# Kernel tuning notes

Hardware: AMD Instinct MI355X
Metric: run time of the kernel (lower is better)

The kernel has to match this reference:

```python
import jax, jax.numpy as jnp
import numpy as np

CLIP = 1.0e6
TRANSITION_JITTER = 1.0e-4
CHOLESKY_JITTER = 1.0e-5
MAX_NLL_PER_STEP = 1.0e4
LOG_2PI = float(np.log(2.0 * np.pi))
T, NUM_SITES, NUM_COMPONENTS = 512, 128, 2
D = NUM_SITES * NUM_COMPONENTS


def _symmetrize(m):
    return 0.5 * (m + m.swapaxes(-1, -2))


def _sanitize_operator(m):
    m = jnp.nan_to_num(m, nan=0.0, posinf=CLIP, neginf=-CLIP)
    return jnp.clip(m, -CLIP, CLIP)


def _sanitize_symmetric(m):
    return _symmetrize(_sanitize_operator(m))


def _sanitize_vector(v):
    v = jnp.nan_to_num(v, nan=0.0, posinf=CLIP, neginf=-CLIP)
    return jnp.clip(v, -CLIP, CLIP)


def setup_inputs() -> dict:
    key = jax.random.key(0)
    ks = jax.random.split(key, 8)
    eye = jnp.eye(D, dtype=jnp.float32)
    # Stable per-step transition: near-identity with small learned-kernel-like perturbation.
    transition = 0.9 * eye + (0.05 / np.sqrt(D)) * jax.random.normal(ks[0], (T, D, D), dtype=jnp.float32)
    forcing = 0.1 * jax.random.normal(ks[1], (T, D), dtype=jnp.float32)
    observations = jax.random.normal(ks[2], (T, D), dtype=jnp.float32)
    # PSD process / measurement covariances (SeparableCrossCovariance outputs are PSD).
    a = jax.random.normal(ks[3], (D, D), dtype=jnp.float32) / np.sqrt(D)
    process_cov = 0.01 * (a @ a.T) + 0.05 * eye
    b = jax.random.normal(ks[4], (D, D), dtype=jnp.float32) / np.sqrt(D)
    measurement_cov = 0.01 * (b @ b.T) + 0.1 * eye
    initial_mean = jax.random.normal(ks[5], (D,), dtype=jnp.float32)
    initial_cov_diag = 0.5 + jax.random.uniform(ks[6], (D,), dtype=jnp.float32)
    return {
        "observations": observations,
        "transition": transition,
        "forcing": forcing,
        "process_cov": process_cov,
        "measurement_cov": measurement_cov,
        "initial_mean": initial_mean,
        "initial_cov_diag": initial_cov_diag,
    }


def reference(observations, transition, forcing, process_cov, measurement_cov, initial_mean, initial_cov_diag):
    dt = observations.dtype
    d = observations.shape[-1]
    eye = jnp.eye(d, dtype=dt)
    Q = _sanitize_symmetric(process_cov) + TRANSITION_JITTER * eye
    R = _sanitize_symmetric(measurement_cov)
    m0 = _sanitize_vector(initial_mean)
    P0 = jnp.diag(jnp.clip(initial_cov_diag, 1e-6, CLIP))

    def step(carry, inp):
        m, P = carry
        A_t, f_t, y_t = inp
        A_t = _sanitize_operator(A_t)
        f_t = _sanitize_vector(f_t)
        # predict
        pred_m = A_t @ m + f_t
        pred_P = _symmetrize(A_t @ P @ A_t.T) + Q
        # innovation (identity measurement operator)
        S = _symmetrize(pred_P + R) + CHOLESKY_JITTER * eye
        L = jnp.linalg.cholesky(S)
        innov = y_t - pred_m
        alpha = jax.scipy.linalg.cho_solve((L, True), innov)      # S^{-1} innov
        K = jax.scipy.linalg.cho_solve((L, True), pred_P).T       # pred_P S^{-1}
        new_m = pred_m + K @ innov
        new_P = _symmetrize((eye - K) @ pred_P)
        logdet = 2.0 * jnp.sum(jnp.log(jnp.diagonal(L)))
        nll_t = 0.5 * (innov @ alpha + logdet + d * LOG_2PI)
        nll_t = jnp.minimum(nll_t, MAX_NLL_PER_STEP)
        return (new_m, new_P), (pred_m, new_m, nll_t)

    (_, _), (pred_means, filt_means, nlls) = jax.lax.scan(
        step, (m0, P0), (transition, forcing, observations)
    )
    return jnp.sum(nlls), filt_means, pred_means
```

## Files before the change

### kernel.cpp

```cpp
#include <hip/hip_runtime.h>
#include <math.h>

#define NWG   65
#define DIM   256
#define LDM   260
#define TSTEPS 512
#define CLIPV 1.0e6f
#define TJIT  1.0e-4f
#define CJIT  1.0e-5f
#define MAXNLL 1.0e4f
#define LOG2PI 1.8378770664093453f

#define OFF_P    0
#define OFF_AP   66560
#define OFF_PP   133120
#define OFF_S    199680
#define OFF_L    266240
#define OFF_GT   332800
#define OFF_SY   399620
#define OFF_Q    466180
#define OFF_R    532740
#define OFF_VEC  599300

__device__ float    g_ws[600832];
__device__ unsigned g_bar[2];
__device__ unsigned g_broken;

__device__ __forceinline__ void gbar() {
    __syncthreads();
    if (threadIdx.x == 0) {
        if (__hip_atomic_load(&g_broken, __ATOMIC_RELAXED, __HIP_MEMORY_SCOPE_AGENT) == 0u) {
            __threadfence();
            unsigned g = __hip_atomic_load(&g_bar[1], __ATOMIC_SEQ_CST, __HIP_MEMORY_SCOPE_AGENT);
            unsigned a = __hip_atomic_fetch_add(&g_bar[0], 1u, __ATOMIC_SEQ_CST, __HIP_MEMORY_SCOPE_AGENT);
            if (a == (unsigned)(NWG - 1)) {
                __hip_atomic_store(&g_bar[0], 0u, __ATOMIC_SEQ_CST, __HIP_MEMORY_SCOPE_AGENT);
                __hip_atomic_fetch_add(&g_bar[1], 1u, __ATOMIC_SEQ_CST, __HIP_MEMORY_SCOPE_AGENT);
            } else {
                int spins = 0;
                while (__hip_atomic_load(&g_bar[1], __ATOMIC_SEQ_CST, __HIP_MEMORY_SCOPE_AGENT) == g) {
                    __builtin_amdgcn_s_sleep(2);
                    if (++spins > 2000000) {
                        __hip_atomic_store(&g_broken, 1u, __ATOMIC_RELAXED, __HIP_MEMORY_SCOPE_AGENT);
                        break;
                    }
                }
            }
            __threadfence();
        }
    }
    __syncthreads();
}

__device__ __forceinline__ float fsan(float x) {
    x = isnan(x) ? 0.0f : x;
    return fminf(fmaxf(x, -CLIPV), CLIPV);
}
__device__ __forceinline__ float rdlane(float v, int l) {
    return __int_as_float(__builtin_amdgcn_readlane(__float_as_int(v), l));
}
__device__ __forceinline__ float wave_sum(float v) {
    #pragma unroll
    for (int off = 32; off; off >>= 1) v += __shfl_xor(v, off, 64);
    return v;
}

__device__ void chol64(const float* src, int sstride, float* Lm, float* rdiag, int b0) {
    const int lane = threadIdx.x & 63;
    float a[64];
    const float* srow = src + (size_t)lane * sstride;
    #pragma unroll
    for (int k = 0; k < 64; k += 4) {
        float4 v = *(const float4*)(srow + k);
        a[k] = v.x; a[k+1] = v.y; a[k+2] = v.z; a[k+3] = v.w;
    }
    float rdv = 0.0f;
    #pragma unroll
    for (int j = 0; j < 64; ++j) {
        float d  = rdlane(a[j], j);
        float sq = sqrtf(d);
        float rs = 1.0f / sq;
        if (lane == j) rdv = rs;
        if (lane >= j) a[j] *= rs;
        float ljrs = a[j] * rs;
        #pragma unroll
        for (int k = j + 1; k < 64; ++k) {
            float skj = rdlane(a[k], j);
            if (lane > j) a[k] = fmaf(-ljrs, skj, a[k]);
        }
    }
    float* lrow = Lm + (size_t)(b0 + lane) * LDM + b0;
    #pragma unroll
    for (int k = 0; k < 64; k += 4) {
        float4 v; v.x = a[k]; v.y = a[k+1]; v.z = a[k+2]; v.w = a[k+3];
        *(float4*)(lrow + k) = v;
    }
    rdiag[b0 + lane] = rdv;
}

__device__ void trsm_col_wave(const float* Sm, float* Lm, const float* rdiag, int b0, int c) {
    const int lane = threadIdx.x & 63;
    float b   = Sm[(size_t)c * LDM + b0 + lane];
    float rdl = rdiag[b0 + lane];
    float x   = 0.0f;
    const float* lbase = Lm + (size_t)(b0 + lane) * LDM + b0;
    for (int i0 = 0; i0 < 64; i0 += 4) {
        float4 lv = *(const float4*)(lbase + i0);
        #pragma unroll
        for (int s = 0; s < 4; ++s) {
            int i = i0 + s;
            float xi = rdlane(b, i) * rdlane(rdl, i);
            x = (lane == i) ? xi : x;
            float lvi = (s == 0) ? lv.x : (s == 1) ? lv.y : (s == 2) ? lv.z : lv.w;
            b = fmaf(-lvi, xi, b);
        }
    }
    Lm[(size_t)c * LDM + b0 + lane] = x;
}

__device__ void gsolve_wave(const float* PPm, const float* innov, float* GT,
                            const float* Lm, const float* rdiag, int c) {
    const int lane = threadIdx.x & 63;
    float b[4], x[4], rd[4];
    const float* lp[4];
    #pragma unroll
    for (int q = 0; q < 4; ++q) {
        int r = lane + 64 * q;
        b[q]  = (c < 256) ? PPm[(size_t)c * LDM + r] : innov[r];
        x[q]  = 0.0f;
        rd[q] = rdiag[r];
        lp[q] = Lm + (size_t)r * LDM;
    }
    #pragma unroll
    for (int q = 0; q < 4; ++q) {
        for (int ii0 = 0; ii0 < 64; ii0 += 4) {
            float4 a0 = *(const float4*)(lp[0] + q * 64 + ii0);
            float4 a1 = *(const float4*)(lp[1] + q * 64 + ii0);
            float4 a2 = *(const float4*)(lp[2] + q * 64 + ii0);
            float4 a3 = *(const float4*)(lp[3] + q * 64 + ii0);
            #pragma unroll
            for (int s = 0; s < 4; ++s) {
                int il = ii0 + s;
                float xi = rdlane(b[q], il) * rdlane(rd[q], il);
                x[q] = (lane == il) ? xi : x[q];
                float c0 = (s==0)?a0.x:(s==1)?a0.y:(s==2)?a0.z:a0.w;
                float c1 = (s==0)?a1.x:(s==1)?a1.y:(s==2)?a1.z:a1.w;
                float c2 = (s==0)?a2.x:(s==1)?a2.y:(s==2)?a2.z:a2.w;
                float c3 = (s==0)?a3.x:(s==1)?a3.y:(s==2)?a3.z:a3.w;
                b[0] = fmaf(-c0, xi, b[0]);
                b[1] = fmaf(-c1, xi, b[1]);
                b[2] = fmaf(-c2, xi, b[2]);
                b[3] = fmaf(-c3, xi, b[3]);
            }
        }
    }
    #pragma unroll
    for (int q = 0; q < 4; ++q) GT[(size_t)c * LDM + lane + 64 * q] = x[q];
}

__device__ void block_update64(float* Sm, const float* Lm, float* smem, int b1, int b0, int tid) {
    float* Ls = smem;
    for (int e = tid; e < 64 * 64; e += 256) {
        int r = e >> 6, k = e & 63;
        Ls[r * 66 + k] = Lm[(size_t)(b1 + r) * LDM + b0 + k];
    }
    __syncthreads();
    int tx = tid & 15, ty = tid >> 4;
    int r0 = 4 * ty, c0 = 4 * tx;
    float acc[4][4] = {};
    for (int k = 0; k < 64; ++k) {
        float xr[4], yc[4];
        #pragma unroll
        for (int q = 0; q < 4; ++q) { xr[q] = Ls[(r0+q)*66 + k]; yc[q] = Ls[(c0+q)*66 + k]; }
        #pragma unroll
        for (int r = 0; r < 4; ++r)
            #pragma unroll
            for (int cc = 0; cc < 4; ++cc) acc[r][cc] = fmaf(xr[r], yc[cc], acc[r][cc]);
    }
    __syncthreads();
    #pragma unroll
    for (int r = 0; r < 4; ++r)
        #pragma unroll
        for (int cc = 0; cc < 4; ++cc)
            Sm[(size_t)(b1 + r0 + r) * LDM + b1 + c0 + cc] -= acc[r][cc];
}

__device__ void trailing_tiles(float* Sm, const float* Lm, float* smem,
                               int rb, int nt, int b0, int wg, int tid) {
    int cnt = 0;
    for (int ti = 0; ti < nt; ++ti) {
        for (int tj = 0; tj <= ti; ++tj) {
            if (ti < 2 && tj < 2) continue;
            if ((cnt++ & 63) != wg) continue;
            int i0 = rb + 32 * ti, j0 = rb + 32 * tj;
            float* Xs = smem;
            float* Ys = smem + 32 * 66;
            for (int e = tid; e < 32 * 64; e += 256) {
                int r = e >> 6, k = e & 63;
                Xs[r * 66 + k] = Lm[(size_t)(i0 + r) * LDM + b0 + k];
                Ys[r * 66 + k] = Lm[(size_t)(j0 + r) * LDM + b0 + k];
            }
            __syncthreads();
            int tx = tid & 15, ty = tid >> 4;
            int r0 = 2 * ty, c0 = 2 * tx;
            float a00 = 0, a01 = 0, a10 = 0, a11 = 0;
            #pragma unroll 4
            for (int k = 0; k < 64; ++k) {
                float x0 = Xs[r0*66 + k], x1 = Xs[(r0+1)*66 + k];
                float y0 = Ys[c0*66 + k], y1 = Ys[(c0+1)*66 + k];
                a00 = fmaf(x0, y0, a00); a01 = fmaf(x0, y1, a01);
                a10 = fmaf(x1, y0, a10); a11 = fmaf(x1, y1, a11);
            }
            __syncthreads();
            int gi = i0 + r0, gj = j0 + c0;
            Sm[(size_t)gi * LDM + gj]           -= a00;
            Sm[(size_t)gi * LDM + gj + 1]       -= a01;
            Sm[(size_t)(gi + 1) * LDM + gj]     -= a10;
            Sm[(size_t)(gi + 1) * LDM + gj + 1] -= a11;
            if (ti != tj) {
                Sm[(size_t)gj * LDM + gi]           -= a00;
                Sm[(size_t)gj * LDM + gi + 1]       -= a10;
                Sm[(size_t)(gj + 1) * LDM + gi]     -= a01;
                Sm[(size_t)(gj + 1) * LDM + gi + 1] -= a11;
            }
        }
    }
}

__global__ __launch_bounds__(256, 1) void kf_kernel(
    const float* __restrict__ obs, const float* __restrict__ trans,
    const float* __restrict__ forc, const float* __restrict__ proc,
    const float* __restrict__ meas, const float* __restrict__ im,
    const float* __restrict__ icd, float* __restrict__ out)
{
    __shared__ float smem[4608];

    const int wg   = blockIdx.x;
    const int tid  = threadIdx.x;
    const int lane = tid & 63;
    const int wv   = tid >> 6;
    const int gw   = wg * 4 + wv;

    float* Pm  = g_ws + OFF_P;
    float* AP  = g_ws + OFF_AP;
    float* PPm = g_ws + OFF_PP;
    float* Sm  = g_ws + OFF_S;
    float* Lm  = g_ws + OFF_L;
    float* GT  = g_ws + OFF_GT;
    float* SY  = g_ws + OFF_SY;
    float* Qm  = g_ws + OFF_Q;
    float* Rm  = g_ws + OFF_R;
    float* vec = g_ws + OFF_VEC;
    float* mvec  = vec;
    float* predm = vec + 256;
    float* innov = vec + 512;
    float* gtz   = vec + 768;
    float* rdiag = vec + 1024;
    float* scal  = vec + 1280;

    float* out_filt = out + 1;
    float* out_pred = out + 1 + TSTEPS * DIM;

    for (int e = wg * 256 + tid; e < DIM * DIM; e += NWG * 256) {
        int i = e >> 8, j = e & 255;
        float q = 0.5f * (fsan(proc[i * 256 + j]) + fsan(proc[j * 256 + i])) + (i == j ? TJIT : 0.0f);
        Qm[(size_t)i * LDM + j] = q;
        Rm[(size_t)i * LDM + j] = 0.5f * (fsan(meas[i * 256 + j]) + fsan(meas[j * 256 + i]));
        Pm[(size_t)i * LDM + j] = (i == j) ? fminf(fmaxf(icd[i], 1e-6f), CLIPV) : 0.0f;
    }
    if (wg == 64) {
        mvec[tid] = fsan(im[tid]);
        gtz[tid]  = 0.0f;
        if (tid < 3) scal[tid] = 0.0f;
    }
    gbar();

    for (int t = 0; t < TSTEPS; ++t) {
        const float* At = trans + (size_t)t * DIM * DIM;

        if (wg < 64) {
            int ti = wg >> 3, tj = wg & 7, i0 = ti * 32, j0 = tj * 32;
            int tx = tid & 15, ty = tid >> 4;
            int r0 = 2 * ty, c0 = 2 * tx;
            float a00 = 0, a01 = 0, a10 = 0, a11 = 0;
            float* As = smem;
            float* Bs = smem + 32 * 66;
            for (int kc = 0; kc < 256; kc += 64) {
                for (int e = tid; e < 32 * 64; e += 256) {
                    int r = e >> 6, k = e & 63;
                    As[r * 66 + k] = fsan(At[(i0 + r) * 256 + kc + k]);
                }
                for (int e = tid; e < 64 * 32; e += 256) {
                    int k = e >> 5, c = e & 31;
                    Bs[k * 34 + c] = Pm[(size_t)(kc + k) * LDM + j0 + c];
                }
                __syncthreads();
                #pragma unroll 8
                for (int k = 0; k < 64; ++k) {
                    float x0 = As[r0*66 + k], x1 = As[(r0+1)*66 + k];
                    float y0 = Bs[k*34 + c0], y1 = Bs[k*34 + c0 + 1];
                    a00 = fmaf(x0, y0, a00); a01 = fmaf(x0, y1, a01);
                    a10 = fmaf(x1, y0, a10); a11 = fmaf(x1, y1, a11);
                }
                __syncthreads();
            }
            AP[(size_t)(i0 + r0) * LDM + j0 + c0]         = a00;
            AP[(size_t)(i0 + r0) * LDM + j0 + c0 + 1]     = a01;
            AP[(size_t)(i0 + r0 + 1) * LDM + j0 + c0]     = a10;
            AP[(size_t)(i0 + r0 + 1) * LDM + j0 + c0 + 1] = a11;
        } else if (t > 0) {
            float nm = predm[tid] + gtz[tid];
            mvec[tid] = nm;
            out_filt[(size_t)(t - 1) * DIM + tid] = nm;
            if (tid == 0) {
                float nll = 0.5f * (scal[0] + scal[1] + 256.0f * LOG2PI);
                scal[2] += fminf(nll, MAXNLL);
            }
        }
        gbar();

        if (wg < 64) {
            int ti = wg >> 3, tj = wg & 7, i0 = ti * 32, j0 = tj * 32;
            int tx = tid & 15, ty = tid >> 4;
            int r0 = 2 * ty, c0 = 2 * tx;
            float a00 = 0, a01 = 0, a10 = 0, a11 = 0;
            float* Xs = smem;
            float* Ys = smem + 32 * 66;
            for (int kc = 0; kc < 256; kc += 64) {
                for (int e = tid; e < 32 * 64; e += 256) {
                    int r = e >> 6, k = e & 63;
                    Xs[r * 66 + k] = AP[(size_t)(i0 + r) * LDM + kc + k];
                    Ys[r * 66 + k] = fsan(At[(j0 + r) * 256 + kc + k]);
                }
                __syncthreads();
                #pragma unroll 8
                for (int k = 0; k < 64; ++k) {
                    float x0 = Xs[r0*66 + k], x1 = Xs[(r0+1)*66 + k];
                    float y0 = Ys[c0*66 + k], y1 = Ys[(c0+1)*66 + k];
                    a00 = fmaf(x0, y0, a00); a01 = fmaf(x0, y1, a01);
                    a10 = fmaf(x1, y0, a10); a11 = fmaf(x1, y1, a11);
                }
                __syncthreads();
            }
            SY[(size_t)(i0 + r0) * LDM + j0 + c0]         = a00;
            SY[(size_t)(i0 + r0) * LDM + j0 + c0 + 1]     = a01;
            SY[(size_t)(i0 + r0 + 1) * LDM + j0 + c0]     = a10;
            SY[(size_t)(i0 + r0 + 1) * LDM + j0 + c0 + 1] = a11;
        }
        gbar();

        if (gw < 256) {
            int r = gw;
            float s = 0.0f;
            #pragma unroll
            for (int q = 0; q < 4; ++q)
                s = fmaf(fsan(At[r * 256 + lane + 64 * q]), mvec[lane + 64 * q], s);
            s = wave_sum(s);
            if (lane == 0) {
                float pm = s + fsan(forc[(size_t)t * DIM + r]);
                predm[r] = pm;
                innov[r] = obs[(size_t)t * DIM + r] - pm;
                out_pred[(size_t)t * DIM + r] = pm;
            }
        }
        if (wg < 64) {
            for (int e = wg * 256 + tid; e < DIM * DIM; e += 64 * 256) {
                int i = e >> 8, j = e & 255;
                float sy = 0.5f * (SY[(size_t)i * LDM + j] + SY[(size_t)j * LDM + i]);
                float pp = sy + Qm[(size_t)i * LDM + j];
                PPm[(size_t)i * LDM + j] = pp;
                Sm[(size_t)i * LDM + j]  = pp + Rm[(size_t)i * LDM + j] + (i == j ? CJIT : 0.0f);
            }
        } else {
            float* Ss = smem;
            for (int e = tid; e < 64 * 64; e += 256) {
                int i = e >> 6, j = e & 63;
                float sy = 0.5f * (SY[(size_t)i * LDM + j] + SY[(size_t)j * LDM + i]);
                Ss[i * 68 + j] = sy + Qm[(size_t)i * LDM + j] + Rm[(size_t)i * LDM + j]
                                 + (i == j ? CJIT : 0.0f);
            }
            __syncthreads();
            if (wv == 0) chol64(Ss, 68, Lm, rdiag, 0);
        }
        gbar();

        if (gw < 192) trsm_col_wave(Sm, Lm, rdiag, 0, 64 + gw);
        gbar();

        if (wg == 64) {
            block_update64(Sm, Lm, smem, 64, 0, tid);
            __syncthreads();
            if (wv == 0) chol64(Sm + (size_t)64 * LDM + 64, LDM, Lm, rdiag, 64);
        } else {
            trailing_tiles(Sm, Lm, smem, 64, 6, 0, wg, tid);
        }
        gbar();

        if (gw < 128) trsm_col_wave(Sm, Lm, rdiag, 64, 128 + gw);
        gbar();

        if (wg == 64) {
            block_update64(Sm, Lm, smem, 128, 64, tid);
            __syncthreads();
            if (wv == 0) chol64(Sm + (size_t)128 * LDM + 128, LDM, Lm, rdiag, 128);
        } else {
            trailing_tiles(Sm, Lm, smem, 128, 4, 64, wg, tid);
        }
        gbar();

        if (gw < 64) trsm_col_wave(Sm, Lm, rdiag, 128, 192 + gw);
        gbar();

        if (wg == 64) {
            block_update64(Sm, Lm, smem, 192, 128, tid);
            __syncthreads();
            if (wv == 0) chol64(Sm + (size_t)192 * LDM + 192, LDM, Lm, rdiag, 192);
        }
        gbar();

        if (gw < 257) gsolve_wave(PPm, innov, GT, Lm, rdiag, gw);
        gbar();

        if (wg < 36) {
            int cnt = 0, ti = 0, tj = 0;
            for (int a = 0; a < 8; ++a)
                for (int b2 = 0; b2 <= a; ++b2) {
                    if (cnt == wg) { ti = a; tj = b2; }
                    ++cnt;
                }
            int i0 = ti * 32, j0 = tj * 32;
            int tx = tid & 15, ty = tid >> 4;
            int r0 = 2 * ty, c0 = 2 * tx;
            float a00 = 0, a01 = 0, a10 = 0, a11 = 0;
            float* Xs = smem;
            float* Ys = smem + 32 * 66;
            for (int kc = 0; kc < 256; kc += 64) {
                for (int e = tid; e < 32 * 64; e += 256) {
                    int r = e >> 6, k = e & 63;
                    Xs[r * 66 + k] = GT[(size_t)(i0 + r) * LDM + kc + k];
                    Ys[r * 66 + k] = GT[(size_t)(j0 + r) * LDM + kc + k];
                }
                __syncthreads();
                #pragma unroll 8
                for (int k = 0; k < 64; ++k) {
                    float x0 = Xs[r0*66 + k], x1 = Xs[(r0+1)*66 + k];
                    float y0 = Ys[c0*66 + k], y1 = Ys[(c0+1)*66 + k];
                    a00 = fmaf(x0, y0, a00); a01 = fmaf(x0, y1, a01);
                    a10 = fmaf(x1, y0, a10); a11 = fmaf(x1, y1, a11);
                }
                __syncthreads();
            }
            int gi = i0 + r0, gj = j0 + c0;
            float v00 = PPm[(size_t)gi * LDM + gj]           - a00;
            float v01 = PPm[(size_t)gi * LDM + gj + 1]       - a01;
            float v10 = PPm[(size_t)(gi + 1) * LDM + gj]     - a10;
            float v11 = PPm[(size_t)(gi + 1) * LDM + gj + 1] - a11;
            Pm[(size_t)gi * LDM + gj]           = v00;
            Pm[(size_t)gi * LDM + gj + 1]       = v01;
            Pm[(size_t)(gi + 1) * LDM + gj]     = v10;
            Pm[(size_t)(gi + 1) * LDM + gj + 1] = v11;
            if (ti != tj) {
                Pm[(size_t)gj * LDM + gi]           = v00;
                Pm[(size_t)gj * LDM + gi + 1]       = v10;
                Pm[(size_t)(gj + 1) * LDM + gi]     = v01;
                Pm[(size_t)(gj + 1) * LDM + gi + 1] = v11;
            }
        } else if (wg < 64) {
            for (int r = gw - 144; r < 256; r += 112) {
                float s = 0.0f;
                #pragma unroll
                for (int q = 0; q < 4; ++q)
                    s = fmaf(GT[(size_t)r * LDM + lane + 64 * q],
                             GT[(size_t)256 * LDM + lane + 64 * q], s);
                s = wave_sum(s);
                if (lane == 0) gtz[r] = s;
            }
        } else {
            if (wv == 0) {
                float s = 0.0f;
                #pragma unroll
                for (int q = 0; q < 4; ++q) {
                    float z = GT[(size_t)256 * LDM + lane + 64 * q];
                    s = fmaf(z, z, s);
                }
                s = wave_sum(s);
                if (lane == 0) scal[0] = s;
            } else if (wv == 1) {
                float s = 0.0f;
                #pragma unroll
                for (int q = 0; q < 4; ++q) s += logf(rdiag[lane + 64 * q]);
                s = wave_sum(s);
                if (lane == 0) scal[1] = -2.0f * s;
            }
        }
        gbar();
    }

    if (wg == 64) {
        float nm = predm[tid] + gtz[tid];
        out_filt[(size_t)511 * DIM + tid] = nm;
        if (tid == 0) {
            float nll = fminf(0.5f * (scal[0] + scal[1] + 256.0f * LOG2PI), MAXNLL);
            out[0] = scal[2] + nll;
            if (__hip_atomic_load(&g_broken, __ATOMIC_RELAXED, __HIP_MEMORY_SCOPE_AGENT) != 0u)
                out[0] = -1.2345678e7f;
        }
    }
}

extern "C" void kernel_launch(void* const* d_in, const int* in_sizes, int n_in,
                              void* d_out, int out_size, void* d_ws, size_t ws_size,
                              hipStream_t stream) {
    (void)in_sizes; (void)n_in; (void)out_size; (void)d_ws; (void)ws_size;
    const float* obs  = (const float*)d_in[0];
    const float* trn  = (const float*)d_in[1];
    const float* forc = (const float*)d_in[2];
    const float* proc = (const float*)d_in[3];
    const float* meas = (const float*)d_in[4];
    const float* im   = (const float*)d_in[5];
    const float* icd  = (const float*)d_in[6];
    float* out = (float*)d_out;

    kf_kernel<<<dim3(NWG), dim3(256), 0, stream>>>(obs, trn, forc, proc, meas, im, icd, out);
}
```

Measured before the change: 157.7 ms.

## Restructure Kalman step: fewer grid barriers, single-block Cholesky, flag-based barrier

Cuts the grid from 65 blocks of 256 threads to 33 blocks of 512. The counter barrier becomes per-block generation flags that every block polls. The A·P·Aᵀ and symmetrize/add stages are fused into one pass that computes both products per tile, and the predicted-mean step is folded into the last block during the A·P phase. The blocked Cholesky, TRSM and trailing updates now run entirely inside one block with __syncthreads instead of grid barriers. This removes many grid-wide barriers per timestep. The cost is serialising the factorisation onto a single CU and having more threads poll flags at each barrier.

```diff
diff --git a/kernel.cpp b/kernel.cpp
--- a/kernel.cpp
+++ b/kernel.cpp
@@ -1,7 +1,9 @@
 #include <hip/hip_runtime.h>
 #include <math.h>
 
-#define NWG   65
+#define NWG   33
+#define NT    512
+#define CHOLW 32
 #define DIM   256
 #define LDM   260
 #define TSTEPS 512
@@ -17,39 +19,36 @@
 #define OFF_S    199680
 #define OFF_L    266240
 #define OFF_GT   332800
-#define OFF_SY   399620
-#define OFF_Q    466180
-#define OFF_R    532740
-#define OFF_VEC  599300
-
-__device__ float    g_ws[600832];
-__device__ unsigned g_bar[2];
+#define OFF_Q    399620
+#define OFF_R    466180
+#define OFF_VEC  532740
+
+__device__ __align__(16) float g_ws[534276];
+struct __align__(128) BarFlag { unsigned v; unsigned pad[31]; };
+__device__ BarFlag g_flags[NWG];
 __device__ unsigned g_broken;
 
-__device__ __forceinline__ void gbar() {
+__device__ __forceinline__ void gbar(unsigned gen) {
     __syncthreads();
     if (threadIdx.x == 0) {
-        if (__hip_atomic_load(&g_broken, __ATOMIC_RELAXED, __HIP_MEMORY_SCOPE_AGENT) == 0u) {
-            __threadfence();
-            unsigned g = __hip_atomic_load(&g_bar[1], __ATOMIC_SEQ_CST, __HIP_MEMORY_SCOPE_AGENT);
-            unsigned a = __hip_atomic_fetch_add(&g_bar[0], 1u, __ATOMIC_SEQ_CST, __HIP_MEMORY_SCOPE_AGENT);
-            if (a == (unsigned)(NWG - 1)) {
-                __hip_atomic_store(&g_bar[0], 0u, __ATOMIC_SEQ_CST, __HIP_MEMORY_SCOPE_AGENT);
-                __hip_atomic_fetch_add(&g_bar[1], 1u, __ATOMIC_SEQ_CST, __HIP_MEMORY_SCOPE_AGENT);
-            } else {
-                int spins = 0;
-                while (__hip_atomic_load(&g_bar[1], __ATOMIC_SEQ_CST, __HIP_MEMORY_SCOPE_AGENT) == g) {
-                    __builtin_amdgcn_s_sleep(2);
-                    if (++spins > 2000000) {
-                        __hip_atomic_store(&g_broken, 1u, __ATOMIC_RELAXED, __HIP_MEMORY_SCOPE_AGENT);
-                        break;
-                    }
-                }
-            }
-            __threadfence();
+        __threadfence();
+        __hip_atomic_store(&g_flags[blockIdx.x].v, gen, __ATOMIC_RELEASE, __HIP_MEMORY_SCOPE_AGENT);
+    }
+    if (threadIdx.x < NWG) {
+        int spins = 0;
+        while (__hip_atomic_load(&g_flags[threadIdx.x].v, __ATOMIC_ACQUIRE, __HIP_MEMORY_SCOPE_AGENT) < gen) {
+            __builtin_amdgcn_s_sleep(1);
+            if (++spins > 4000000) {
+                __hip_atomic_store(&g_broken, 1u, __ATOMIC_RELAXED, __HIP_MEMORY_SCOPE_AGENT);
+                break;
+            }
+            if ((spins & 2047) == 0 &&
+                __hip_atomic_load(&g_broken, __ATOMIC_RELAXED, __HIP_MEMORY_SCOPE_AGENT) != 0u)
+                break;
         }
     }
     __syncthreads();
+    __threadfence();
 }
 
 __device__ __forceinline__ float fsan(float x) {
@@ -65,6 +64,7 @@
     return v;
 }
 
+__attribute__((noinline))
 __device__ void chol64(const float* src, int sstride, float* Lm, float* rdiag, int b0) {
     const int lane = threadIdx.x & 63;
     float a[64];
@@ -78,15 +78,13 @@
     #pragma unroll
     for (int j = 0; j < 64; ++j) {
         float d  = rdlane(a[j], j);
-        float sq = sqrtf(d);
-        float rs = 1.0f / sq;
+        float rs = 1.0f / sqrtf(d);
         if (lane == j) rdv = rs;
         if (lane >= j) a[j] *= rs;
-        float ljrs = a[j] * rs;
         #pragma unroll
         for (int k = j + 1; k < 64; ++k) {
-            float skj = rdlane(a[k], j);
-            if (lane > j) a[k] = fmaf(-ljrs, skj, a[k]);
+            float lkj = rdlane(a[j], k);
+            if (lane > j) a[k] = fmaf(-a[j], lkj, a[k]);
         }
     }
     float* lrow = Lm + (size_t)(b0 + lane) * LDM + b0;
@@ -158,88 +156,59 @@
     for (int q = 0; q < 4; ++q) GT[(size_t)c * LDM + lane + 64 * q] = x[q];
 }
 
-__device__ void block_update64(float* Sm, const float* Lm, float* smem, int b1, int b0, int tid) {
-    float* Ls = smem;
-    for (int e = tid; e < 64 * 64; e += 256) {
-        int r = e >> 6, k = e & 63;
-        Ls[r * 66 + k] = Lm[(size_t)(b1 + r) * LDM + b0 + k];
-    }
-    __syncthreads();
-    int tx = tid & 15, ty = tid >> 4;
-    int r0 = 4 * ty, c0 = 4 * tx;
+__device__ void trail_tile_wave(float* Sm, const float* Lm, int i0, int j0, int b0) {
+    const int lane = threadIdx.x & 63;
+    const int ly = lane >> 3, lx = lane & 7;
     float acc[4][4] = {};
-    for (int k = 0; k < 64; ++k) {
-        float xr[4], yc[4];
-        #pragma unroll
-        for (int q = 0; q < 4; ++q) { xr[q] = Ls[(r0+q)*66 + k]; yc[q] = Ls[(c0+q)*66 + k]; }
+    for (int kk = 0; kk < 64; kk += 4) {
+        float4 xv[4], yv[4];
+        #pragma unroll
+        for (int r = 0; r < 4; ++r)
+            xv[r] = *(const float4*)(Lm + (size_t)(i0 + 4*ly + r) * LDM + b0 + kk);
+        #pragma unroll
+        for (int c = 0; c < 4; ++c)
+            yv[c] = *(const float4*)(Lm + (size_t)(j0 + 4*lx + c) * LDM + b0 + kk);
         #pragma unroll
         for (int r = 0; r < 4; ++r)
             #pragma unroll
-            for (int cc = 0; cc < 4; ++cc) acc[r][cc] = fmaf(xr[r], yc[cc], acc[r][cc]);
-    }
-    __syncthreads();
+            for (int c = 0; c < 4; ++c) {
+                acc[r][c] = fmaf(xv[r].x, yv[c].x, acc[r][c]);
+                acc[r][c] = fmaf(xv[r].y, yv[c].y, acc[r][c]);
+                acc[r][c] = fmaf(xv[r].z, yv[c].z, acc[r][c]);
+                acc[r][c] = fmaf(xv[r].w, yv[c].w, acc[r][c]);
+            }
+    }
     #pragma unroll
     for (int r = 0; r < 4; ++r)
         #pragma unroll
-        for (int cc = 0; cc < 4; ++cc)
-            Sm[(size_t)(b1 + r0 + r) * LDM + b1 + c0 + cc] -= acc[r][cc];
-}
-
-__device__ void trailing_tiles(float* Sm, const float* Lm, float* smem,
-                               int rb, int nt, int b0, int wg, int tid) {
-    int cnt = 0;
-    for (int ti = 0; ti < nt; ++ti) {
-        for (int tj = 0; tj <= ti; ++tj) {
-            if (ti < 2 && tj < 2) continue;
-            if ((cnt++ & 63) != wg) continue;
-            int i0 = rb + 32 * ti, j0 = rb + 32 * tj;
-            float* Xs = smem;
-            float* Ys = smem + 32 * 66;
-            for (int e = tid; e < 32 * 64; e += 256) {
-                int r = e >> 6, k = e & 63;
-                Xs[r * 66 + k] = Lm[(size_t)(i0 + r) * LDM + b0 + k];
-                Ys[r * 66 + k] = Lm[(size_t)(j0 + r) * LDM + b0 + k];
-            }
-            __syncthreads();
-            int tx = tid & 15, ty = tid >> 4;
-            int r0 = 2 * ty, c0 = 2 * tx;
-            float a00 = 0, a01 = 0, a10 = 0, a11 = 0;
-            #pragma unroll 4
-            for (int k = 0; k < 64; ++k) {
-                float x0 = Xs[r0*66 + k], x1 = Xs[(r0+1)*66 + k];
-                float y0 = Ys[c0*66 + k], y1 = Ys[(c0+1)*66 + k];
-                a00 = fmaf(x0, y0, a00); a01 = fmaf(x0, y1, a01);
-                a10 = fmaf(x1, y0, a10); a11 = fmaf(x1, y1, a11);
-            }
-            __syncthreads();
-            int gi = i0 + r0, gj = j0 + c0;
-            Sm[(size_t)gi * LDM + gj]           -= a00;
-            Sm[(size_t)gi * LDM + gj + 1]       -= a01;
-            Sm[(size_t)(gi + 1) * LDM + gj]     -= a10;
-            Sm[(size_t)(gi + 1) * LDM + gj + 1] -= a11;
-            if (ti != tj) {
-                Sm[(size_t)gj * LDM + gi]           -= a00;
-                Sm[(size_t)gj * LDM + gi + 1]       -= a10;
-                Sm[(size_t)(gj + 1) * LDM + gi]     -= a01;
-                Sm[(size_t)(gj + 1) * LDM + gi + 1] -= a11;
-            }
-        }
-    }
-}
-
-__global__ __launch_bounds__(256, 1) void kf_kernel(
+        for (int c = 0; c < 4; ++c)
+            Sm[(size_t)(i0 + 4*ly + r) * LDM + j0 + 4*lx + c] -= acc[r][c];
+}
+
+__device__ void trail_panel(float* Sm, const float* Lm, int rb, int nt, int b0, int wv) {
+    const int cnt = nt * (nt + 1) / 2;
+    for (int idx = wv; idx < cnt; idx += 8) {
+        int ti = 0, tj = 0;
+        for (int a = 0, s = 0; a < nt; ++a) {
+            if (idx < s + a + 1) { ti = a; tj = idx - s; break; }
+            s += a + 1;
+        }
+        trail_tile_wave(Sm, Lm, rb + 32 * ti, rb + 32 * tj, b0);
+    }
+}
+
+__global__ __launch_bounds__(NT, 2) void kf_kernel(
     const float* __restrict__ obs, const float* __restrict__ trans,
     const float* __restrict__ forc, const float* __restrict__ proc,
     const float* __restrict__ meas, const float* __restrict__ im,
     const float* __restrict__ icd, float* __restrict__ out)
 {
-    __shared__ float smem[4608];
+    __shared__ float smem[8576];
 
     const int wg   = blockIdx.x;
     const int tid  = threadIdx.x;
     const int lane = tid & 63;
     const int wv   = tid >> 6;
-    const int gw   = wg * 4 + wv;
 
     float* Pm  = g_ws + OFF_P;
     float* AP  = g_ws + OFF_AP;
@@ -247,7 +216,6 @@
     float* Sm  = g_ws + OFF_S;
     float* Lm  = g_ws + OFF_L;
     float* GT  = g_ws + OFF_GT;
-    float* SY  = g_ws + OFF_SY;
     float* Qm  = g_ws + OFF_Q;
     float* Rm  = g_ws + OFF_R;
     float* vec = g_ws + OFF_VEC;
@@ -261,44 +229,47 @@
     float* out_filt = out + 1;
     float* out_pred = out + 1 + TSTEPS * DIM;
 
-    for (int e = wg * 256 + tid; e < DIM * DIM; e += NWG * 256) {
+    unsigned gen = __hip_atomic_load(&g_flags[blockIdx.x].v, __ATOMIC_RELAXED, __HIP_MEMORY_SCOPE_AGENT);
+
+    for (int e = wg * NT + tid; e < DIM * DIM; e += NWG * NT) {
         int i = e >> 8, j = e & 255;
-        float q = 0.5f * (fsan(proc[i * 256 + j]) + fsan(proc[j * 256 + i])) + (i == j ? TJIT : 0.0f);
-        Qm[(size_t)i * LDM + j] = q;
+        Qm[(size_t)i * LDM + j] = 0.5f * (fsan(proc[i * 256 + j]) + fsan(proc[j * 256 + i]))
+                                  + (i == j ? TJIT : 0.0f);
         Rm[(size_t)i * LDM + j] = 0.5f * (fsan(meas[i * 256 + j]) + fsan(meas[j * 256 + i]));
         Pm[(size_t)i * LDM + j] = (i == j) ? fminf(fmaxf(icd[i], 1e-6f), CLIPV) : 0.0f;
     }
-    if (wg == 64) {
+    if (wg == CHOLW && tid < 256) {
         mvec[tid] = fsan(im[tid]);
         gtz[tid]  = 0.0f;
         if (tid < 3) scal[tid] = 0.0f;
     }
-    gbar();
+    gbar(++gen);
 
     for (int t = 0; t < TSTEPS; ++t) {
         const float* At = trans + (size_t)t * DIM * DIM;
 
-        if (wg < 64) {
-            int ti = wg >> 3, tj = wg & 7, i0 = ti * 32, j0 = tj * 32;
-            int tx = tid & 15, ty = tid >> 4;
-            int r0 = 2 * ty, c0 = 2 * tx;
+        if (wg < 32) {
+            const int ti = wg >> 2, tj = wg & 3;
+            const int i0 = ti * 32, j0 = tj * 64;
+            const int ty = tid >> 5, tx = tid & 31;
+            const int r0 = 2 * ty, c0 = 2 * tx;
             float a00 = 0, a01 = 0, a10 = 0, a11 = 0;
             float* As = smem;
-            float* Bs = smem + 32 * 66;
+            float* Bs = smem + 32 * 68;
             for (int kc = 0; kc < 256; kc += 64) {
-                for (int e = tid; e < 32 * 64; e += 256) {
+                for (int e = tid; e < 32 * 64; e += NT) {
                     int r = e >> 6, k = e & 63;
-                    As[r * 66 + k] = fsan(At[(i0 + r) * 256 + kc + k]);
-                }
-                for (int e = tid; e < 64 * 32; e += 256) {
-                    int k = e >> 5, c = e & 31;
-                    Bs[k * 34 + c] = Pm[(size_t)(kc + k) * LDM + j0 + c];
+                    As[r * 68 + k] = fsan(At[(i0 + r) * 256 + kc + k]);
+                }
+                for (int e = tid; e < 64 * 64; e += NT) {
+                    int r = e >> 6, c = e & 63;
+                    Bs[r * 68 + c] = Pm[(size_t)(kc + r) * LDM + j0 + c];
                 }
                 __syncthreads();
                 #pragma unroll 8
                 for (int k = 0; k < 64; ++k) {
-                    float x0 = As[r0*66 + k], x1 = As[(r0+1)*66 + k];
-                    float y0 = Bs[k*34 + c0], y1 = Bs[k*34 + c0 + 1];
+                    float x0 = As[r0 * 68 + k], x1 = As[(r0 + 1) * 68 + k];
+                    float y0 = Bs[k * 68 + c0], y1 = Bs[k * 68 + c0 + 1];
                     a00 = fmaf(x0, y0, a00); a01 = fmaf(x0, y1, a01);
                     a10 = fmaf(x1, y0, a10); a11 = fmaf(x1, y1, a11);
                 }
@@ -308,179 +279,161 @@
             AP[(size_t)(i0 + r0) * LDM + j0 + c0 + 1]     = a01;
             AP[(size_t)(i0 + r0 + 1) * LDM + j0 + c0]     = a10;
             AP[(size_t)(i0 + r0 + 1) * LDM + j0 + c0 + 1] = a11;
-        } else if (t > 0) {
-            float nm = predm[tid] + gtz[tid];
-            mvec[tid] = nm;
-            out_filt[(size_t)(t - 1) * DIM + tid] = nm;
-            if (tid == 0) {
-                float nll = 0.5f * (scal[0] + scal[1] + 256.0f * LOG2PI);
-                scal[2] += fminf(nll, MAXNLL);
-            }
-        }
-        gbar();
-
-        if (wg < 64) {
-            int ti = wg >> 3, tj = wg & 7, i0 = ti * 32, j0 = tj * 32;
-            int tx = tid & 15, ty = tid >> 4;
-            int r0 = 2 * ty, c0 = 2 * tx;
-            float a00 = 0, a01 = 0, a10 = 0, a11 = 0;
-            float* Xs = smem;
-            float* Ys = smem + 32 * 66;
-            for (int kc = 0; kc < 256; kc += 64) {
-                for (int e = tid; e < 32 * 64; e += 256) {
-                    int r = e >> 6, k = e & 63;
-                    Xs[r * 66 + k] = AP[(size_t)(i0 + r) * LDM + kc + k];
-                    Ys[r * 66 + k] = fsan(At[(j0 + r) * 256 + kc + k]);
-                }
-                __syncthreads();
-                #pragma unroll 8
-                for (int k = 0; k < 64; ++k) {
-                    float x0 = Xs[r0*66 + k], x1 = Xs[(r0+1)*66 + k];
-                    float y0 = Ys[c0*66 + k], y1 = Ys[(c0+1)*66 + k];
-                    a00 = fmaf(x0, y0, a00); a01 = fmaf(x0, y1, a01);
-                    a10 = fmaf(x1, y0, a10); a11 = fmaf(x1, y1, a11);
-                }
-                __syncthreads();
-            }
-            SY[(size_t)(i0 + r0) * LDM + j0 + c0]         = a00;
-            SY[(size_t)(i0 + r0) * LDM + j0 + c0 + 1]     = a01;
-            SY[(size_t)(i0 + r0 + 1) * LDM + j0 + c0]     = a10;
-            SY[(size_t)(i0 + r0 + 1) * LDM + j0 + c0 + 1] = a11;
-        }
-        gbar();
-
-        if (gw < 256) {
-            int r = gw;
-            float s = 0.0f;
-            #pragma unroll
-            for (int q = 0; q < 4; ++q)
-                s = fmaf(fsan(At[r * 256 + lane + 64 * q]), mvec[lane + 64 * q], s);
-            s = wave_sum(s);
-            if (lane == 0) {
-                float pm = s + fsan(forc[(size_t)t * DIM + r]);
-                predm[r] = pm;
-                innov[r] = obs[(size_t)t * DIM + r] - pm;
-                out_pred[(size_t)t * DIM + r] = pm;
-            }
-        }
-        if (wg < 64) {
-            for (int e = wg * 256 + tid; e < DIM * DIM; e += 64 * 256) {
-                int i = e >> 8, j = e & 255;
-                float sy = 0.5f * (SY[(size_t)i * LDM + j] + SY[(size_t)j * LDM + i]);
-                float pp = sy + Qm[(size_t)i * LDM + j];
-                PPm[(size_t)i * LDM + j] = pp;
-                Sm[(size_t)i * LDM + j]  = pp + Rm[(size_t)i * LDM + j] + (i == j ? CJIT : 0.0f);
-            }
         } else {
-            float* Ss = smem;
-            for (int e = tid; e < 64 * 64; e += 256) {
-                int i = e >> 6, j = e & 63;
-                float sy = 0.5f * (SY[(size_t)i * LDM + j] + SY[(size_t)j * LDM + i]);
-                Ss[i * 68 + j] = sy + Qm[(size_t)i * LDM + j] + Rm[(size_t)i * LDM + j]
-                                 + (i == j ? CJIT : 0.0f);
-            }
-            __syncthreads();
-            if (wv == 0) chol64(Ss, 68, Lm, rdiag, 0);
-        }
-        gbar();
-
-        if (gw < 192) trsm_col_wave(Sm, Lm, rdiag, 0, 64 + gw);
-        gbar();
-
-        if (wg == 64) {
-            block_update64(Sm, Lm, smem, 64, 0, tid);
-            __syncthreads();
-            if (wv == 0) chol64(Sm + (size_t)64 * LDM + 64, LDM, Lm, rdiag, 64);
-        } else {
-            trailing_tiles(Sm, Lm, smem, 64, 6, 0, wg, tid);
-        }
-        gbar();
-
-        if (gw < 128) trsm_col_wave(Sm, Lm, rdiag, 64, 128 + gw);
-        gbar();
-
-        if (wg == 64) {
-            block_update64(Sm, Lm, smem, 128, 64, tid);
-            __syncthreads();
-            if (wv == 0) chol64(Sm + (size_t)128 * LDM + 128, LDM, Lm, rdiag, 128);
-        } else {
-            trailing_tiles(Sm, Lm, smem, 128, 4, 64, wg, tid);
-        }
-        gbar();
-
-        if (gw < 64) trsm_col_wave(Sm, Lm, rdiag, 128, 192 + gw);
-        gbar();
-
-        if (wg == 64) {
-            block_update64(Sm, Lm, smem, 192, 128, tid);
-            __syncthreads();
-            if (wv == 0) chol64(Sm + (size_t)192 * LDM + 192, LDM, Lm, rdiag, 192);
-        }
-        gbar();
-
-        if (gw < 257) gsolve_wave(PPm, innov, GT, Lm, rdiag, gw);
-        gbar();
-
-        if (wg < 36) {
-            int cnt = 0, ti = 0, tj = 0;
-            for (int a = 0; a < 8; ++a)
-                for (int b2 = 0; b2 <= a; ++b2) {
-                    if (cnt == wg) { ti = a; tj = b2; }
-                    ++cnt;
-                }
-            int i0 = ti * 32, j0 = tj * 32;
-            int tx = tid & 15, ty = tid >> 4;
-            int r0 = 2 * ty, c0 = 2 * tx;
-            float a00 = 0, a01 = 0, a10 = 0, a11 = 0;
-            float* Xs = smem;
-            float* Ys = smem + 32 * 66;
-            for (int kc = 0; kc < 256; kc += 64) {
-                for (int e = tid; e < 32 * 64; e += 256) {
-                    int r = e >> 6, k = e & 63;
-                    Xs[r * 66 + k] = GT[(size_t)(i0 + r) * LDM + kc + k];
-                    Ys[r * 66 + k] = GT[(size_t)(j0 + r) * LDM + kc + k];
-                }
-                __syncthreads();
-                #pragma unroll 8
-                for (int k = 0; k < 64; ++k) {
-                    float x0 = Xs[r0*66 + k], x1 = Xs[(r0+1)*66 + k];
-                    float y0 = Ys[c0*66 + k], y1 = Ys[(c0+1)*66 + k];
-                    a00 = fmaf(x0, y0, a00); a01 = fmaf(x0, y1, a01);
-                    a10 = fmaf(x1, y0, a10); a11 = fmaf(x1, y1, a11);
-                }
-                __syncthreads();
-            }
-            int gi = i0 + r0, gj = j0 + c0;
-            float v00 = PPm[(size_t)gi * LDM + gj]           - a00;
-            float v01 = PPm[(size_t)gi * LDM + gj + 1]       - a01;
-            float v10 = PPm[(size_t)(gi + 1) * LDM + gj]     - a10;
-            float v11 = PPm[(size_t)(gi + 1) * LDM + gj + 1] - a11;
-            Pm[(size_t)gi * LDM + gj]           = v00;
-            Pm[(size_t)gi * LDM + gj + 1]       = v01;
-            Pm[(size_t)(gi + 1) * LDM + gj]     = v10;
-            Pm[(size_t)(gi + 1) * LDM + gj + 1] = v11;
-            if (ti != tj) {
-                Pm[(size_t)gj * LDM + gi]           = v00;
-                Pm[(size_t)gj * LDM + gi + 1]       = v10;
-                Pm[(size_t)(gj + 1) * LDM + gi]     = v01;
-                Pm[(size_t)(gj + 1) * LDM + gi + 1] = v11;
-            }
-        } else if (wg < 64) {
-            for (int r = gw - 144; r < 256; r += 112) {
+            if (t > 0 && tid < 256) {
+                float nm = predm[tid] + gtz[tid];
+                mvec[tid] = nm;
+                out_filt[(size_t)(t - 1) * DIM + tid] = nm;
+                if (tid == 0) {
+                    float nll = 0.5f * (scal[0] + scal[1] + 256.0f * LOG2PI);
+                    scal[2] += fminf(nll, MAXNLL);
+                }
+            }
+            __syncthreads();
+            for (int r = wv * 32; r < wv * 32 + 32; ++r) {
                 float s = 0.0f;
                 #pragma unroll
                 for (int q = 0; q < 4; ++q)
-                    s = fmaf(GT[(size_t)r * LDM + lane + 64 * q],
-                             GT[(size_t)256 * LDM + lane + 64 * q], s);
+                    s = fmaf(fsan(At[(size_t)r * 256 + lane + 64 * q]), mvec[lane + 64 * q], s);
+                s = wave_sum(s);
+                if (lane == 0) {
+                    float pm = s + fsan(forc[(size_t)t * DIM + r]);
+                    predm[r] = pm;
+                    innov[r] = obs[(size_t)t * DIM + r] - pm;
+                    out_pred[(size_t)t * DIM + r] = pm;
+                }
+            }
+        }
+        gbar(++gen);
+
+        for (int idx = wg; idx < 36; idx += NWG) {
+            int ti = 0, tj = 0;
+            for (int a = 0, s = 0; a < 8; ++a) {
+                if (idx < s + a + 1) { ti = a; tj = idx - s; break; }
+                s += a + 1;
+            }
+            const int i0 = 32 * ti, j0 = 32 * tj;
+            const int ty = tid >> 5, tx = tid & 31;
+            const int r0 = 2 * ty;
+            float acc1_0 = 0, acc1_1 = 0, acc2_0 = 0, acc2_1 = 0;
+            float* APi = smem;
+            float* Aj  = smem + 32 * 67;
+            float* Ai  = smem + 2 * 32 * 67;
+            float* APj = smem + 3 * 32 * 67;
+            for (int kc = 0; kc < 256; kc += 64) {
+                for (int e = tid; e < 32 * 64; e += NT) {
+                    int r = e >> 6, k = e & 63;
+                    APi[r * 67 + k] = AP[(size_t)(i0 + r) * LDM + kc + k];
+                    Aj [r * 67 + k] = fsan(At[(j0 + r) * 256 + kc + k]);
+                    Ai [r * 67 + k] = fsan(At[(i0 + r) * 256 + kc + k]);
+                    APj[r * 67 + k] = AP[(size_t)(j0 + r) * LDM + kc + k];
+                }
+                __syncthreads();
+                #pragma unroll 4
+                for (int k = 0; k < 64; ++k) {
+                    float aj  = Aj [tx * 67 + k];
+                    float apj = APj[tx * 67 + k];
+                    float x0 = APi[r0 * 67 + k], x1 = APi[(r0 + 1) * 67 + k];
+                    float w0 = Ai [r0 * 67 + k], w1 = Ai [(r0 + 1) * 67 + k];
+                    acc1_0 = fmaf(x0, aj,  acc1_0); acc1_1 = fmaf(x1, aj,  acc1_1);
+                    acc2_0 = fmaf(w0, apj, acc2_0); acc2_1 = fmaf(w1, apj, acc2_1);
+                }
+                __syncthreads();
+            }
+            #pragma unroll
+            for (int r = 0; r < 2; ++r) {
+                int gi = i0 + r0 + r, gj = j0 + tx;
+                float sym = 0.5f * ((r == 0 ? acc1_0 : acc1_1) + (r == 0 ? acc2_0 : acc2_1));
+                float pp  = sym + Qm[(size_t)gi * LDM + gj];
+                PPm[(size_t)gi * LDM + gj] = pp;
+                PPm[(size_t)gj * LDM + gi] = pp;
+                if (gi >= gj)
+                    Sm[(size_t)gi * LDM + gj] = pp + Rm[(size_t)gi * LDM + gj]
+                                                + (gi == gj ? CJIT : 0.0f);
+            }
+        }
+        gbar(++gen);
+
+        if (wg == CHOLW) {
+            if (wv == 0) chol64(Sm, LDM, Lm, rdiag, 0);
+            __syncthreads();
+            for (int c = 64 + wv; c < 256; c += 8) trsm_col_wave(Sm, Lm, rdiag, 0, c);
+            __syncthreads();
+            trail_panel(Sm, Lm, 64, 6, 0, wv);
+            __syncthreads();
+            if (wv == 0) chol64(Sm + (size_t)64 * LDM + 64, LDM, Lm, rdiag, 64);
+            __syncthreads();
+            for (int c = 128 + wv; c < 256; c += 8) trsm_col_wave(Sm, Lm, rdiag, 64, c);
+            __syncthreads();
+            trail_panel(Sm, Lm, 128, 4, 64, wv);
+            __syncthreads();
+            if (wv == 0) chol64(Sm + (size_t)128 * LDM + 128, LDM, Lm, rdiag, 128);
+            __syncthreads();
+            for (int c = 192 + wv; c < 256; c += 8) trsm_col_wave(Sm, Lm, rdiag, 128, c);
+            __syncthreads();
+            trail_panel(Sm, Lm, 192, 2, 128, wv);
+            __syncthreads();
+            if (wv == 0) chol64(Sm + (size_t)192 * LDM + 192, LDM, Lm, rdiag, 192);
+        }
+        gbar(++gen);
+
+        {
+            int c = wg * 8 + wv;
+            if (c < 257) gsolve_wave(PPm, innov, GT, Lm, rdiag, c);
+        }
+        gbar(++gen);
+
+        if (wg < 32) {
+            for (int idx = wg; idx < 36; idx += 32) {
+                int ti = 0, tj = 0;
+                for (int a = 0, s = 0; a < 8; ++a) {
+                    if (idx < s + a + 1) { ti = a; tj = idx - s; break; }
+                    s += a + 1;
+                }
+                const int i0 = 32 * ti, j0 = 32 * tj;
+                const int ty = tid >> 5, tx = tid & 31;
+                const int r0 = 2 * ty;
+                float acc0 = 0, acc1 = 0;
+                float* GTi = smem;
+                float* GTj = smem + 32 * 67;
+                for (int kc = 0; kc < 256; kc += 64) {
+                    for (int e = tid; e < 32 * 64; e += NT) {
+                        int r = e >> 6, k = e & 63;
+                        GTi[r * 67 + k] = GT[(size_t)(i0 + r) * LDM + kc + k];
+                        GTj[r * 67 + k] = GT[(size_t)(j0 + r) * LDM + kc + k];
+                    }
+                    __syncthreads();
+                    #pragma unroll 4
+                    for (int k = 0; k < 64; ++k) {
+                        float gj = GTj[tx * 67 + k];
+                        acc0 = fmaf(GTi[r0 * 67 + k],       gj, acc0);
+                        acc1 = fmaf(GTi[(r0 + 1) * 67 + k], gj, acc1);
+                    }
+                    __syncthreads();
+                }
+                #pragma unroll
+                for (int r = 0; r < 2; ++r) {
+                    int gi = i0 + r0 + r, gj = j0 + tx;
+                    float v = PPm[(size_t)gi * LDM + gj] - (r == 0 ? acc0 : acc1);
+                    Pm[(size_t)gi * LDM + gj] = v;
+                    Pm[(size_t)gj * LDM + gi] = v;
+                }
+            }
+        } else {
+            const float* zrow = GT + (size_t)256 * LDM;
+            for (int r = wv * 32; r < wv * 32 + 32; ++r) {
+                float s = 0.0f;
+                #pragma unroll
+                for (int q = 0; q < 4; ++q)
+                    s = fmaf(GT[(size_t)r * LDM + lane + 64 * q], zrow[lane + 64 * q], s);
                 s = wave_sum(s);
                 if (lane == 0) gtz[r] = s;
             }
-        } else {
             if (wv == 0) {
                 float s = 0.0f;
                 #pragma unroll
                 for (int q = 0; q < 4; ++q) {
-                    float z = GT[(size_t)256 * LDM + lane + 64 * q];
+                    float z = zrow[lane + 64 * q];
                     s = fmaf(z, z, s);
                 }
                 s = wave_sum(s);
@@ -493,10 +446,10 @@
                 if (lane == 0) scal[1] = -2.0f * s;
             }
         }
-        gbar();
-    }
-
-    if (wg == 64) {
+        gbar(++gen);
+    }
+
+    if (wg == CHOLW && tid < 256) {
         float nm = predm[tid] + gtz[tid];
         out_filt[(size_t)511 * DIM + tid] = nm;
         if (tid == 0) {
@@ -521,5 +474,5 @@
     const float* icd  = (const float*)d_in[6];
     float* out = (float*)d_out;
 
-    kf_kernel<<<dim3(NWG), dim3(256), 0, stream>>>(obs, trn, forc, proc, meas, im, icd, out);
-}
+    kf_kernel<<<dim3(NWG), dim3(NT), 0, stream>>>(obs, trn, forc, proc, meas, im, icd, out);
+}
```

Measured after the change: 382.7 ms. 143% more time.
